# Performance work log

Measured on AMD Instinct MI355X. Metric: run time of the kernel, lower is better.

## Reference

```python
import jax, jax.numpy as jnp
import numpy as np

B, H, W, C, NUM_HEADS = 32, 8, 128, 512, 8
HK, WK = 7, 11  # local_k
N = H * W
HEAD_DIM = C // NUM_HEADS
SCALE = HEAD_DIM ** (-0.5)


def make_local_mask():
    # key (i,j) is visible to query (h,w) iff i+HK//2 in [h, h+HK) and j+WK//2 in [w, w+WK)
    dh = jnp.arange(H)[None, :] - jnp.arange(H)[:, None] + HK // 2  # [H(query), H(key)]
    dw = jnp.arange(W)[None, :] - jnp.arange(W)[:, None] + WK // 2  # [W(query), W(key)]
    ok_h = (dh >= 0) & (dh < HK)
    ok_w = (dw >= 0) & (dw < WK)
    ok = ok_h[:, None, :, None] & ok_w[None, :, None, :]  # [H,W,H,W]
    return jnp.where(ok.reshape(N, N), 0.0, -jnp.inf).astype(jnp.float32)


def setup_inputs() -> dict:
    key = jax.random.key(0)
    k1, k2, k3 = jax.random.split(key, 3)
    s = C ** (-0.5)
    return {
        "x": jax.random.normal(k1, (B, N, C), dtype=jnp.float32),
        "w_qkv": jax.random.normal(k2, (C, 3 * C), dtype=jnp.float32) * s,
        "w_proj": jax.random.normal(k3, (C, C), dtype=jnp.float32) * s,
        "b_proj": jnp.zeros((C,), dtype=jnp.float32),
    }


def reference(x, w_qkv, w_proj, b_proj):
    mask = make_local_mask()  # [N, N], 0 in window, -inf outside
    b, n, c = x.shape
    qkv = (x @ w_qkv).reshape(b, n, 3, NUM_HEADS, HEAD_DIM)
    qkv = jnp.transpose(qkv, (2, 0, 3, 1, 4))  # [3, B, heads, N, head_dim]
    q, k, v = qkv[0], qkv[1], qkv[2]
    attn = jnp.einsum('bhqd,bhkd->bhqk', q, k) * SCALE + mask
    attn = jax.nn.softmax(attn, axis=-1)
    out = jnp.einsum('bhqk,bhkd->bhqd', attn, v)
    out = jnp.transpose(out, (0, 2, 1, 3)).reshape(b, n, c)
    return out @ w_proj + b_proj
```

## Files before the change

### kernel.cpp

```cpp
#include <hip/hip_runtime.h>

#define Bsz   32
#define Hh    8
#define Ww    128
#define Cc    512
#define NHEAD 8
#define HD    64
#define NN    1024
#define SCALE 0.125f
#define ROWS  1536

typedef _Float16 f16x8 __attribute__((ext_vector_type(8)));
typedef float    f32x4 __attribute__((ext_vector_type(4)));

__device__ __forceinline__ void gload16(const _Float16* g, _Float16* l) {
#if __has_builtin(__builtin_amdgcn_global_load_lds)
  __builtin_amdgcn_global_load_lds(
      (const __attribute__((address_space(1))) unsigned int*)g,
      (__attribute__((address_space(3))) unsigned int*)l, 16, 0, 0);
#else
  *(uint4*)l = *(const uint4*)g;
#endif
}

__global__ __launch_bounds__(256) void cvt_f32_f16(
    const float* __restrict__ in, _Float16* __restrict__ out, int n8) {
  const int i = blockIdx.x * 256 + threadIdx.x;
  if (i < n8) {
    const float4 f0 = ((const float4*)in)[(size_t)i * 2];
    const float4 f1 = ((const float4*)in)[(size_t)i * 2 + 1];
    union { _Float16 h[8]; uint4 u; } pk;
    pk.h[0] = (_Float16)f0.x; pk.h[1] = (_Float16)f0.y;
    pk.h[2] = (_Float16)f0.z; pk.h[3] = (_Float16)f0.w;
    pk.h[4] = (_Float16)f1.x; pk.h[5] = (_Float16)f1.y;
    pk.h[6] = (_Float16)f1.z; pk.h[7] = (_Float16)f1.w;
    ((uint4*)out)[i] = pk.u;
  }
}

__global__ __launch_bounds__(256) void tcvt(
    const float* __restrict__ in, _Float16* __restrict__ out, int Nn, int K) {
  const int id = blockIdx.x * 256 + threadIdx.x;
  if (id < Nn * K) {
    const int n = id / K, k = id - n * K;
    out[id] = (_Float16)in[(size_t)k * Nn + n];
  }
}

template<bool OUT_F16, bool HAS_BIAS>
__global__ __launch_bounds__(512, 4) void gemm_mfma(
    const _Float16* __restrict__ A,
    const _Float16* __restrict__ BT,
    const float* __restrict__ bias,
    void* __restrict__ Cout,
    int nbx, int Nn, int K)
{
  __shared__ _Float16 As[2][128 * 32];
  __shared__ _Float16 Bs[2][256 * 32];

  const int wg    = blockIdx.x;
  const int chunk = gridDim.x >> 3;
  const int nid   = (wg & 7) * chunk + (wg >> 3);
  const int bn    = (nid % nbx) * 256;
  const int bm    = (nid / nbx) * 128;

  const int t  = threadIdx.x;
  const int l  = t & 63, wv = t >> 6;
  const int wr = wv >> 2, wc = wv & 3;

  f32x4 acc[4][4] = {};

  const int arow = t >> 2;
  const int ac   = (t & 3) * 8;

  auto stage = [&](int k0, int pb) {
    gload16(A  + (size_t)(bm + arow)       * K + k0 + ac, &As[pb][arow * 32 + ac]);
    gload16(BT + (size_t)(bn + arow)       * K + k0 + ac, &Bs[pb][arow * 32 + ac]);
    gload16(BT + (size_t)(bn + 128 + arow) * K + k0 + ac, &Bs[pb][(128 + arow) * 32 + ac]);
  };

  const int nt = K / 32;

  stage(0, 0);
  __syncthreads();

  int buf = 0;
  for (int tt = 0; tt < nt; ++tt) {
    if (tt + 1 < nt) stage((tt + 1) * 32, buf ^ 1);

    const int rA = l & 15, ks = (l >> 4) * 8;
    f16x8 aF[4], bF[4];
#pragma unroll
    for (int i = 0; i < 4; ++i)
      aF[i] = *(const f16x8*)&As[buf][(wr * 64 + i * 16 + rA) * 32 + ks];
#pragma unroll
    for (int j = 0; j < 4; ++j)
      bF[j] = *(const f16x8*)&Bs[buf][(wc * 64 + j * 16 + rA) * 32 + ks];
#pragma unroll
    for (int i = 0; i < 4; ++i)
#pragma unroll
      for (int j = 0; j < 4; ++j)
        acc[i][j] = __builtin_amdgcn_mfma_f32_16x16x32_f16(aF[i], bF[j], acc[i][j], 0, 0, 0);

    __syncthreads();
    buf ^= 1;
  }

  const int lc = l & 15, lr4 = (l >> 4) * 4;
#pragma unroll
  for (int i = 0; i < 4; ++i) {
    const size_t row0 = (size_t)(bm + wr * 64 + i * 16 + lr4);
#pragma unroll
    for (int j = 0; j < 4; ++j) {
      const int col = bn + wc * 64 + j * 16 + lc;
      const float bv = HAS_BIAS ? bias[col] : 0.f;
#pragma unroll
      for (int r = 0; r < 4; ++r) {
        const float v = acc[i][j][r] + bv;
        if (OUT_F16)
          ((_Float16*)Cout)[(row0 + r) * Nn + col] = (_Float16)v;
        else
          ((float*)Cout)[(row0 + r) * Nn + col] = v;
      }
    }
  }
}

__global__ __launch_bounds__(512, 4) void local_attn_mfma(
    const _Float16* __restrict__ qkv, _Float16* __restrict__ outh)
{
  const int wg  = blockIdx.x + (Hh / 2) * (blockIdx.y + NHEAD * blockIdx.z);
  const int nid = ((wg & 7) << 7) + (wg >> 3);
  const int hp = nid & 3, head = (nid >> 2) & 7, b = nid >> 5;
  const int h0 = hp * 2;

  const int t = threadIdx.x;
  const int wv = t >> 6, l = t & 63;
  const int g = l >> 4, c = l & 15;
  const int w0 = wv * 16;
  const int kb = min(max(w0 - 8, 0), 96);

  __shared__ _Float16 Vsh[64 * 132];
  __shared__ _Float16 Pbuf[8][576];

  const _Float16* qb = qkv + (size_t)b * NN * ROWS;

  f16x8 qF[2][2];
#pragma unroll
  for (int hi = 0; hi < 2; ++hi) {
    const _Float16* Qg = qb + (size_t)((h0 + hi) * Ww + w0 + c) * ROWS + head * HD;
    qF[hi][0] = *(const f16x8*)&Qg[g * 8];
    qF[hi][1] = *(const f16x8*)&Qg[32 + g * 8];
  }

  float mbias[2][4];
#pragma unroll
  for (int tt = 0; tt < 2; ++tt)
#pragma unroll
    for (int r = 0; r < 4; ++r) {
      const int kcol = kb + 16 * tt + 4 * g + r;
      const int qq   = w0 + c;
      mbias[tt][r] = (kcol >= qq - 5 && kcol <= qq + 5) ? 0.f : -1e30f;
    }

  const int r0 = max(0, h0 - 3), r1 = min(Hh - 1, h0 + 4);
  float m_run[2] = {-1e30f, -1e30f}, s_run[2] = {0.f, 0.f};
  f32x4 accO[2][4] = {};

  const int dd = t & 7, cg = (t & 255) >> 3;

  for (int kr = r0; kr <= r1; ++kr) {
    __syncthreads();
    if (t < 256) {
      f16x8 vr[4];
      const _Float16* Vg = qb + (size_t)(kr * Ww + cg * 4) * ROWS + 2 * Cc + head * HD + dd * 8;
#pragma unroll
      for (int i = 0; i < 4; ++i)
        vr[i] = *(const f16x8*)&Vg[(size_t)i * ROWS];
#pragma unroll
      for (int e = 0; e < 8; ++e) {
        union { _Float16 hh[4]; uint2 u; } pk;
        pk.hh[0] = vr[0][e]; pk.hh[1] = vr[1][e];
        pk.hh[2] = vr[2][e]; pk.hh[3] = vr[3][e];
        *(uint2*)&Vsh[(dd * 8 + e) * 132 + cg * 4] = pk.u;
      }
    }
    __syncthreads();

    const _Float16* Kg = qb + (size_t)(kr * Ww) * ROWS + Cc + head * HD;

#pragma unroll
    for (int hi = 0; hi < 2; ++hi) {
      const int hq = h0 + hi;
      if (kr < hq - 3 || kr > hq + 3) continue;

      f32x4 accS[2] = {};
#pragma unroll
      for (int tt = 0; tt < 2; ++tt) {
        const int col = kb + 16 * tt + c;
#pragma unroll
        for (int s = 0; s < 2; ++s) {
          const f16x8 kF = *(const f16x8*)&Kg[(size_t)col * ROWS + (s * 4 + g) * 8];
          accS[tt] = __builtin_amdgcn_mfma_f32_16x16x32_f16(kF, qF[hi][s], accS[tt], 0, 0, 0);
        }
      }

      float sc[2][4];
      float smax = -1e30f;
#pragma unroll
      for (int tt = 0; tt < 2; ++tt)
#pragma unroll
        for (int r = 0; r < 4; ++r) {
          sc[tt][r] = __builtin_fmaf(accS[tt][r], SCALE, mbias[tt][r]);
          smax = fmaxf(smax, sc[tt][r]);
        }
      smax = fmaxf(smax, __shfl_xor(smax, 16));
      smax = fmaxf(smax, __shfl_xor(smax, 32));
      const float mnew  = fmaxf(m_run[hi], smax);
      const float alpha = __expf(m_run[hi] - mnew);
      m_run[hi] = mnew;

      float ps = 0.f;
#pragma unroll
      for (int tt = 0; tt < 2; ++tt) {
        float p0 = __expf(sc[tt][0] - mnew), p1 = __expf(sc[tt][1] - mnew);
        float p2 = __expf(sc[tt][2] - mnew), p3 = __expf(sc[tt][3] - mnew);
        ps += (p0 + p1) + (p2 + p3);
        union { _Float16 hh[4]; uint2 u; } pk;
        pk.hh[0] = (_Float16)p0; pk.hh[1] = (_Float16)p1;
        pk.hh[2] = (_Float16)p2; pk.hh[3] = (_Float16)p3;
        *(uint2*)&Pbuf[wv][c * 36 + 16 * tt + 4 * g] = pk.u;
      }
      ps += __shfl_xor(ps, 16);
      ps += __shfl_xor(ps, 32);
      s_run[hi] = s_run[hi] * alpha + ps;

      float alr[4];
#pragma unroll
      for (int r = 0; r < 4; ++r)
        alr[r] = __shfl(alpha, 4 * g + r, 16);

      asm volatile("s_waitcnt lgkmcnt(0)" ::: "memory");

      union { f16x8 v; uint2 u2[2]; } pF;
      {
        const _Float16* pp = &Pbuf[wv][c * 36 + g * 8];
        pF.u2[0] = *(const uint2*)pp;
        pF.u2[1] = *(const uint2*)(pp + 4);
      }
#pragma unroll
      for (int jj = 0; jj < 4; ++jj)
#pragma unroll
        for (int r = 0; r < 4; ++r) accO[hi][jj][r] *= alr[r];
#pragma unroll
      for (int jj = 0; jj < 4; ++jj) {
        union { f16x8 v; uint2 u2[2]; } vF;
        const _Float16* vp = &Vsh[(16 * jj + c) * 132 + kb + g * 8];
        vF.u2[0] = *(const uint2*)vp;
        vF.u2[1] = *(const uint2*)(vp + 4);
        accO[hi][jj] = __builtin_amdgcn_mfma_f32_16x16x32_f16(pF.v, vF.v, accO[hi][jj], 0, 0, 0);
      }
    }
  }

#pragma unroll
  for (int hi = 0; hi < 2; ++hi) {
    _Float16* ob = outh + ((size_t)b * NN + (h0 + hi) * Ww + w0) * Cc + head * HD;
#pragma unroll
    for (int r = 0; r < 4; ++r) {
      const float sr  = __shfl(s_run[hi], 4 * g + r, 16);
      const float inv = 1.f / sr;
      const int q = 4 * g + r;
#pragma unroll
      for (int jj = 0; jj < 4; ++jj)
        ob[(size_t)q * Cc + 16 * jj + c] = (_Float16)(accO[hi][jj][r] * inv);
    }
  }
}

extern "C" void kernel_launch(void* const* d_in, const int* in_sizes, int n_in,
                              void* d_out, int out_size, void* d_ws, size_t ws_size,
                              hipStream_t stream)
{
  const float* x      = (const float*)d_in[0];
  const float* w_qkv  = (const float*)d_in[1];
  const float* w_proj = (const float*)d_in[2];
  const float* b_proj = (const float*)d_in[3];
  float* out = (float*)d_out;

  const int M = Bsz * NN;
  char* ws = (char*)d_ws;
  _Float16* xh    = (_Float16*)ws;
  _Float16* qkvh  = (_Float16*)(ws + 33554432);
  _Float16* attnh = (_Float16*)(ws + 134217728);
  _Float16* wqT   = (_Float16*)(ws + 167772160);
  _Float16* wpT   = (_Float16*)(ws + 167772160 + 1572864);

  cvt_f32_f16<<<(M * Cc / 8 + 255) / 256, 256, 0, stream>>>(x, xh, M * Cc / 8);
  tcvt<<<(ROWS * Cc + 255) / 256, 256, 0, stream>>>(w_qkv, wqT, ROWS, Cc);
  tcvt<<<(Cc * Cc + 255) / 256, 256, 0, stream>>>(w_proj, wpT, Cc, Cc);

  gemm_mfma<true, false><<<(ROWS / 256) * (M / 128), 512, 0, stream>>>(
      xh, wqT, nullptr, qkvh, ROWS / 256, ROWS, Cc);

  local_attn_mfma<<<dim3(Hh / 2, NHEAD, Bsz), 512, 0, stream>>>(qkvh, attnh);

  gemm_mfma<false, true><<<(Cc / 256) * (M / 128), 512, 0, stream>>>(
      attnh, wpT, b_proj, out, Cc / 256, Cc, Cc);
}
```

Measured before the change: 196.0 us.

## Write V transposed from QKV GEMM epilogue and read it directly in attention

The QKV GEMM epilogue now writes the V columns into a separate per-(batch,head) transposed buffer [d][token]. The attention kernel no longer stages and transposes V through shared memory with two barriers per key row. Instead it loads V fragments straight from global memory. It also raises wave priority around the MFMA blocks and reuses the x buffer for the attention output. The cost is scattered 2-byte stores in the GEMM epilogue and uncached global V loads in the attention loop.

```diff
diff --git a/kernel.cpp b/kernel.cpp
--- a/kernel.cpp
+++ b/kernel.cpp
@@ -47,12 +47,13 @@
   }
 }
 
-template<bool OUT_F16, bool HAS_BIAS>
+template<bool QKV_SPLIT, bool OUT_F16, bool HAS_BIAS>
 __global__ __launch_bounds__(512, 4) void gemm_mfma(
     const _Float16* __restrict__ A,
     const _Float16* __restrict__ BT,
     const float* __restrict__ bias,
     void* __restrict__ Cout,
+    _Float16* __restrict__ vt,
     int nbx, int Nn, int K)
 {
   __shared__ _Float16 As[2][128 * 32];
@@ -114,20 +115,32 @@
     for (int j = 0; j < 4; ++j) {
       const int col = bn + wc * 64 + j * 16 + lc;
       const float bv = HAS_BIAS ? bias[col] : 0.f;
-#pragma unroll
-      for (int r = 0; r < 4; ++r) {
-        const float v = acc[i][j][r] + bv;
-        if (OUT_F16)
-          ((_Float16*)Cout)[(row0 + r) * Nn + col] = (_Float16)v;
-        else
-          ((float*)Cout)[(row0 + r) * Nn + col] = v;
+      if (QKV_SPLIT && col >= 2 * Cc) {
+        const int head = (col - 2 * Cc) >> 6;
+        const int d    = (col - 2 * Cc) & 63;
+#pragma unroll
+        for (int r = 0; r < 4; ++r) {
+          const size_t row = row0 + r;
+          const size_t bh  = (row >> 10) * NHEAD + head;
+          vt[(bh * HD + d) * NN + (row & 1023)] = (_Float16)acc[i][j][r];
+        }
+      } else {
+#pragma unroll
+        for (int r = 0; r < 4; ++r) {
+          const float v = acc[i][j][r] + bv;
+          if (OUT_F16)
+            ((_Float16*)Cout)[(row0 + r) * Nn + col] = (_Float16)v;
+          else
+            ((float*)Cout)[(row0 + r) * Nn + col] = v;
+        }
       }
     }
   }
 }
 
 __global__ __launch_bounds__(512, 4) void local_attn_mfma(
-    const _Float16* __restrict__ qkv, _Float16* __restrict__ outh)
+    const _Float16* __restrict__ qkv, const _Float16* __restrict__ vt,
+    _Float16* __restrict__ outh)
 {
   const int wg  = blockIdx.x + (Hh / 2) * (blockIdx.y + NHEAD * blockIdx.z);
   const int nid = ((wg & 7) << 7) + (wg >> 3);
@@ -140,10 +153,10 @@
   const int w0 = wv * 16;
   const int kb = min(max(w0 - 8, 0), 96);
 
-  __shared__ _Float16 Vsh[64 * 132];
   __shared__ _Float16 Pbuf[8][576];
 
   const _Float16* qb = qkv + (size_t)b * NN * ROWS;
+  const _Float16* Vt = vt + ((size_t)b * NHEAD + head) * HD * NN;
 
   f16x8 qF[2][2];
 #pragma unroll
@@ -167,27 +180,9 @@
   float m_run[2] = {-1e30f, -1e30f}, s_run[2] = {0.f, 0.f};
   f32x4 accO[2][4] = {};
 
-  const int dd = t & 7, cg = (t & 255) >> 3;
-
   for (int kr = r0; kr <= r1; ++kr) {
-    __syncthreads();
-    if (t < 256) {
-      f16x8 vr[4];
-      const _Float16* Vg = qb + (size_t)(kr * Ww + cg * 4) * ROWS + 2 * Cc + head * HD + dd * 8;
-#pragma unroll
-      for (int i = 0; i < 4; ++i)
-        vr[i] = *(const f16x8*)&Vg[(size_t)i * ROWS];
-#pragma unroll
-      for (int e = 0; e < 8; ++e) {
-        union { _Float16 hh[4]; uint2 u; } pk;
-        pk.hh[0] = vr[0][e]; pk.hh[1] = vr[1][e];
-        pk.hh[2] = vr[2][e]; pk.hh[3] = vr[3][e];
-        *(uint2*)&Vsh[(dd * 8 + e) * 132 + cg * 4] = pk.u;
-      }
-    }
-    __syncthreads();
-
     const _Float16* Kg = qb + (size_t)(kr * Ww) * ROWS + Cc + head * HD;
+    const _Float16* Vk = Vt + kr * Ww + kb;
 
 #pragma unroll
     for (int hi = 0; hi < 2; ++hi) {
@@ -195,6 +190,7 @@
       if (kr < hq - 3 || kr > hq + 3) continue;
 
       f32x4 accS[2] = {};
+      __builtin_amdgcn_s_setprio(1);
 #pragma unroll
       for (int tt = 0; tt < 2; ++tt) {
         const int col = kb + 16 * tt + c;
@@ -204,6 +200,7 @@
           accS[tt] = __builtin_amdgcn_mfma_f32_16x16x32_f16(kF, qF[hi][s], accS[tt], 0, 0, 0);
         }
       }
+      __builtin_amdgcn_s_setprio(0);
 
       float sc[2][4];
       float smax = -1e30f;
@@ -252,14 +249,13 @@
       for (int jj = 0; jj < 4; ++jj)
 #pragma unroll
         for (int r = 0; r < 4; ++r) accO[hi][jj][r] *= alr[r];
+      __builtin_amdgcn_s_setprio(1);
 #pragma unroll
       for (int jj = 0; jj < 4; ++jj) {
-        union { f16x8 v; uint2 u2[2]; } vF;
-        const _Float16* vp = &Vsh[(16 * jj + c) * 132 + kb + g * 8];
-        vF.u2[0] = *(const uint2*)vp;
-        vF.u2[1] = *(const uint2*)(vp + 4);
-        accO[hi][jj] = __builtin_amdgcn_mfma_f32_16x16x32_f16(pF.v, vF.v, accO[hi][jj], 0, 0, 0);
-      }
+        const f16x8 vF = *(const f16x8*)&Vk[(size_t)(16 * jj + c) * NN + 8 * g];
+        accO[hi][jj] = __builtin_amdgcn_mfma_f32_16x16x32_f16(pF.v, vF, accO[hi][jj], 0, 0, 0);
+      }
+      __builtin_amdgcn_s_setprio(0);
     }
   }
 
@@ -291,8 +287,9 @@
   const int M = Bsz * NN;
   char* ws = (char*)d_ws;
   _Float16* xh    = (_Float16*)ws;
+  _Float16* attnh = (_Float16*)ws;
   _Float16* qkvh  = (_Float16*)(ws + 33554432);
-  _Float16* attnh = (_Float16*)(ws + 134217728);
+  _Float16* vt    = (_Float16*)(ws + 134217728);
   _Float16* wqT   = (_Float16*)(ws + 167772160);
   _Float16* wpT   = (_Float16*)(ws + 167772160 + 1572864);
 
@@ -300,11 +297,11 @@
   tcvt<<<(ROWS * Cc + 255) / 256, 256, 0, stream>>>(w_qkv, wqT, ROWS, Cc);
   tcvt<<<(Cc * Cc + 255) / 256, 256, 0, stream>>>(w_proj, wpT, Cc, Cc);
 
-  gemm_mfma<true, false><<<(ROWS / 256) * (M / 128), 512, 0, stream>>>(
-      xh, wqT, nullptr, qkvh, ROWS / 256, ROWS, Cc);
-
-  local_attn_mfma<<<dim3(Hh / 2, NHEAD, Bsz), 512, 0, stream>>>(qkvh, attnh);
-
-  gemm_mfma<false, true><<<(Cc / 256) * (M / 128), 512, 0, stream>>>(
-      attnh, wpT, b_proj, out, Cc / 256, Cc, Cc);
-}
+  gemm_mfma<true, true, false><<<(ROWS / 256) * (M / 128), 512, 0, stream>>>(
+      xh, wqT, nullptr, qkvh, vt, ROWS / 256, ROWS, Cc);
+
+  local_attn_mfma<<<dim3(Hh / 2, NHEAD, Bsz), 512, 0, stream>>>(qkvh, vt, attnh);
+
+  gemm_mfma<false, false, true><<<(Cc / 256) * (M / 128), 512, 0, stream>>>(
+      attnh, wpT, b_proj, out, nullptr, Cc / 256, Cc, Cc);
+}
```

Result: slower. 227.0 us (+15.8%).
